# Kernel optimization log

Measured on AMD Instinct MI355X. Metric: run time of the kernel, lower is better.

Reference implementation:

```python
import jax, jax.numpy as jnp
import numpy as np
from jax import lax

B, H, W = 8, 512, 512


def setup_inputs() -> dict:
    key = jax.random.key(0)
    k1, k2, k3, k4, k5 = jax.random.split(key, 5)
    img = jax.random.uniform(k1, (B, 3, H, W), jnp.float32)
    omega = 0.8 + 0.15 * jax.random.uniform(k2, (B, 1), jnp.float32)
    atmospheric_light = 0.5 + 0.5 * jax.random.uniform(k3, (B, 3), jnp.float32)
    L_low = 2.0 * jax.random.uniform(k4, (B, 1), jnp.float32)          # percent in [0,2)
    L_high = 95.0 + 4.0 * jax.random.uniform(k5, (B, 1), jnp.float32)  # percent in [95,99)
    guided_radius = 15  # python int, uniform across batch (original clamps to [1,50])
    return {"img": img, "omega": omega, "atmospheric_light": atmospheric_light,
            "L_low": L_low, "L_high": L_high, "guided_radius": guided_radius}


def _box_filter(x, r):
    # reflect-pad + mean over (2r+1)x(2r+1) window, separable (exactly avg_pool2d on reflect-padded input)
    k = 2 * r + 1
    xp = jnp.pad(x, ((0, 0), (0, 0), (r, r), (r, r)), mode='reflect')
    s = lax.reduce_window(xp, 0.0, lax.add, (1, 1, k, 1), (1, 1, 1, 1), 'VALID')
    s = lax.reduce_window(s, 0.0, lax.add, (1, 1, 1, k), (1, 1, 1, 1), 'VALID')
    return s / (k * k)


def _forward(img, omega, atmospheric_light, L_low, L_high, r):
    eps = 0.5
    Bb, Cc, Hh, Ww = img.shape
    A = atmospheric_light.reshape(Bb, 3, 1, 1)
    # initial transmission: t = 1 - omega * min_c(I/A)
    dark = jnp.min(img / (A + 1e-8), axis=1, keepdims=True)           # (B,1,H,W)
    t0 = 1.0 - omega.reshape(Bb, 1, 1, 1) * dark
    # gradient constraint (weights from t0, applied to shifted copies)
    wx = jnp.exp(-jnp.abs(t0[:, :, :, 1:] - t0[:, :, :, :-1]))
    tx = jnp.concatenate([t0[:, :, :, :1], t0[:, :, :, :-1] * wx], axis=3)
    wy = jnp.exp(-jnp.abs(t0[:, :, 1:, :] - t0[:, :, :-1, :]))
    tg = jnp.concatenate([tx[:, :, :1, :], tx[:, :, :-1, :] * wy], axis=2)
    # guided filter with grayscale guide
    rgb_w = jnp.array([0.299, 0.587, 0.114], dtype=img.dtype).reshape(1, 3, 1, 1)
    gray = jnp.sum(img * rgb_w, axis=1, keepdims=True)                # (B,1,H,W)
    mI = _box_filter(gray, r)
    mp = _box_filter(tg, r)
    mIp = _box_filter(gray * tg, r)
    cov_Ip = mIp - mI * mp
    var_I = _box_filter(gray * gray, r) - mI * mI
    a = cov_Ip / (var_I + eps)
    b = mp - a * mI
    t_final = jnp.clip(_box_filter(a, r) * gray + _box_filter(b, r), 0.1, 1.0)
    # restoration
    J = jnp.clip((img - A) / (t_final + 1e-8) + A, 0.0, 1.0)
    # percentile color stretch (vectorized over B and C)
    n = Hh * Ww
    svals = jnp.sort(J.reshape(Bb, Cc, n), axis=-1)
    li = jnp.clip((L_low / 100.0 * n).astype(jnp.int32), 0, n - 1)    # (B,1)
    hi = jnp.clip((L_high / 100.0 * n).astype(jnp.int32), 0, n - 1)
    p_low = jnp.take_along_axis(svals, jnp.broadcast_to(li[:, :, None], (Bb, Cc, 1)), axis=-1).reshape(Bb, Cc, 1, 1)
    p_high = jnp.take_along_axis(svals, jnp.broadcast_to(hi[:, :, None], (Bb, Cc, 1)), axis=-1).reshape(Bb, Cc, 1, 1)
    out = (jnp.clip(J, p_low, p_high) - p_low) / (p_high - p_low + 1e-8)
    return jnp.clip(out, 0.0, 1.0)


def reference(img, omega, atmospheric_light, L_low, L_high, guided_radius):
    r = max(1, min(int(guided_radius), 50))
    return _forward(img, omega, atmospheric_light, L_low, L_high, r)
```

## Files before the change

### kernel.cpp

```cpp
#include <hip/hip_runtime.h>
#include <cstdint>

constexpr int Bb = 8, Hh = 512, Ww = 512;
constexpr int HWn = Hh * Ww;
constexpr int CHK2 = 16;
constexpr int CHK4 = 16;
constexpr int NBIN = 2048;

__device__ __forceinline__ int reflect_idx(int p, int n) {
    p = (p < 0) ? -p : p;
    return (p < n) ? p : (2 * n - 2 - p);
}
__device__ __forceinline__ int clamp_r(const int* rad) {
    int r = rad[0];
    return (r < 1) ? 1 : ((r > 50) ? 50 : r);
}

__global__ __launch_bounds__(512) void k1_stats_h(
    const float* __restrict__ img, const float* __restrict__ omega,
    const float* __restrict__ atm, const int* __restrict__ rad,
    float4* __restrict__ hq, unsigned int* __restrict__ histzero)
{
    const int i = blockIdx.x;
    const int b = blockIdx.y;
    const int j = threadIdx.x;
    const int fbid = b * gridDim.x + i;
    if (fbid < 96) histzero[fbid * 512 + j] = 0u;
    const int r = clamp_r(rad);

    __shared__ float t0c[512], t0p[512];
    __shared__ float4 Pb[512];
    __shared__ float4 wsum[8];

    const float om = omega[b];
    const float iA0 = 1.0f / (atm[b*3+0] + 1e-8f);
    const float iA1 = 1.0f / (atm[b*3+1] + 1e-8f);
    const float iA2 = 1.0f / (atm[b*3+2] + 1e-8f);
    const float* imb = img + (size_t)b * 3 * HWn;
    const int ip = (i > 0) ? (i - 1) : 0;

    float r0 = imb[0*HWn + i*Ww + j];
    float g0 = imb[1*HWn + i*Ww + j];
    float b0 = imb[2*HWn + i*Ww + j];
    t0c[j] = 1.0f - om * fminf(fminf(r0*iA0, g0*iA1), b0*iA2);
    float r1 = imb[0*HWn + ip*Ww + j];
    float g1 = imb[1*HWn + ip*Ww + j];
    float b1 = imb[2*HWn + ip*Ww + j];
    t0p[j] = 1.0f - om * fminf(fminf(r1*iA0, g1*iA1), b1*iA2);
    float gr = 0.299f*r0 + 0.587f*g0 + 0.114f*b0;
    __syncthreads();

    float tx = (j == 0) ? t0p[0] : t0p[j-1] * __expf(-fabsf(t0p[j] - t0p[j-1]));
    float tgv = (i == 0) ? tx : tx * __expf(-fabsf(t0c[j] - t0p[j]));

    const int lane = j & 63, wv = j >> 6;
    float4 incl;
    incl.x = gr; incl.y = tgv; incl.z = gr * tgv; incl.w = gr * gr;
    #pragma unroll
    for (int off = 1; off < 64; off <<= 1) {
        float ux = __shfl_up(incl.x, off);
        float uy = __shfl_up(incl.y, off);
        float uz = __shfl_up(incl.z, off);
        float uw = __shfl_up(incl.w, off);
        if (lane >= off) { incl.x += ux; incl.y += uy; incl.z += uz; incl.w += uw; }
    }
    if (lane == 63) wsum[wv] = incl;
    __syncthreads();
    float4 o4; o4.x = 0.f; o4.y = 0.f; o4.z = 0.f; o4.w = 0.f;
    #pragma unroll
    for (int w = 0; w < 7; ++w) {
        if (w < wv) {
            float4 t = wsum[w];
            o4.x += t.x; o4.y += t.y; o4.z += t.z; o4.w += t.w;
        }
    }
    float4 P; P.x = incl.x + o4.x; P.y = incl.y + o4.y; P.z = incl.z + o4.z; P.w = incl.w + o4.w;
    Pb[j] = P;
    __syncthreads();

    const int lo = j - r, hi = j + r;
    float4 s = Pb[(hi > 511) ? 511 : hi];
    if (lo > 0) {
        float4 t = Pb[lo-1];
        s.x -= t.x; s.y -= t.y; s.z -= t.z; s.w -= t.w;
    }
    if (lo < 0) {
        float4 t = Pb[r - j], u = Pb[0];
        s.x += t.x - u.x; s.y += t.y - u.y; s.z += t.z - u.z; s.w += t.w - u.w;
    }
    if (hi > 511) {
        float4 t = Pb[510], u = Pb[1021 - j - r];
        s.x += t.x - u.x; s.y += t.y - u.y; s.z += t.z - u.z; s.w += t.w - u.w;
    }
    hq[((size_t)b * Hh + i) * Ww + j] = s;
}

__global__ __launch_bounds__(256) void k2_stats_v(
    const float4* __restrict__ hq, const int* __restrict__ rad,
    float2* __restrict__ ab)
{
    const int b  = blockIdx.y;
    const int y0 = blockIdx.x * CHK2;
    const int j  = blockIdx.z * 256 + threadIdx.x;
    const int r  = clamp_r(rad);
    const float ikk = 1.0f / (float)((2*r+1) * (2*r+1));

    float4 s; s.x = 0.f; s.y = 0.f; s.z = 0.f; s.w = 0.f;
    for (int d = -r; d <= r; ++d) {
        int m = reflect_idx(y0 + d, Hh);
        float4 v = hq[((size_t)b * Hh + m) * Ww + j];
        s.x += v.x; s.y += v.y; s.z += v.z; s.w += v.w;
    }
    for (int y = y0; y < y0 + CHK2; ++y) {
        float mI = s.x * ikk, mp = s.y * ikk, mIp = s.z * ikk, mII = s.w * ikk;
        float av = (mIp - mI * mp) / (mII - mI * mI + 0.5f);
        float bv = mp - av * mI;
        float2 o; o.x = av; o.y = bv;
        ab[((size_t)b * Hh + y) * Ww + j] = o;
        int yin  = reflect_idx(y + 1 + r, Hh);
        int yout = reflect_idx(y - r, Hh);
        float4 vi = hq[((size_t)b * Hh + yin)  * Ww + j];
        float4 vo = hq[((size_t)b * Hh + yout) * Ww + j];
        s.x += vi.x - vo.x; s.y += vi.y - vo.y; s.z += vi.z - vo.z; s.w += vi.w - vo.w;
    }
}

__global__ __launch_bounds__(512) void k3_ab_h(
    const float2* __restrict__ ab, const int* __restrict__ rad,
    float2* __restrict__ hab)
{
    const int i = blockIdx.x;
    const int b = blockIdx.y;
    const int j = threadIdx.x;
    const int r = clamp_r(rad);
    const int lane = j & 63, wv = j >> 6;

    __shared__ float2 Pb[512];
    __shared__ float2 wsum[8];

    float2 v = ab[((size_t)b * Hh + i) * Ww + j];
    float2 incl = v;
    #pragma unroll
    for (int off = 1; off < 64; off <<= 1) {
        float ux = __shfl_up(incl.x, off);
        float uy = __shfl_up(incl.y, off);
        if (lane >= off) { incl.x += ux; incl.y += uy; }
    }
    if (lane == 63) wsum[wv] = incl;
    __syncthreads();
    float ox = 0.f, oy = 0.f;
    #pragma unroll
    for (int w = 0; w < 7; ++w) {
        if (w < wv) { float2 t = wsum[w]; ox += t.x; oy += t.y; }
    }
    float2 P; P.x = incl.x + ox; P.y = incl.y + oy;
    Pb[j] = P;
    __syncthreads();

    const int lo = j - r, hi = j + r;
    float2 s = Pb[(hi > 511) ? 511 : hi];
    if (lo > 0)   { float2 t = Pb[lo-1];  s.x -= t.x; s.y -= t.y; }
    if (lo < 0)   { float2 t = Pb[r-j], u = Pb[0];
                    s.x += t.x - u.x; s.y += t.y - u.y; }
    if (hi > 511) { float2 t = Pb[510], u = Pb[1021-j-r];
                    s.x += t.x - u.x; s.y += t.y - u.y; }
    hab[((size_t)b * Hh + i) * Ww + j] = s;
}

__global__ __launch_bounds__(256) void k4_final_v(
    const float2* __restrict__ hab, const float* __restrict__ img,
    const float* __restrict__ atm, const int* __restrict__ rad,
    float* __restrict__ J, unsigned int* __restrict__ hist)
{
    const int b  = blockIdx.y;
    const int y0 = blockIdx.x * CHK4;
    const int j  = blockIdx.z * 256 + threadIdx.x;
    const int tid = threadIdx.x;
    const int r  = clamp_r(rad);
    const float ikk = 1.0f / (float)((2*r+1) * (2*r+1));

    __shared__ unsigned int lh[3][NBIN];
    for (int t = tid; t < 3 * NBIN; t += 256) ((unsigned int*)lh)[t] = 0u;
    __syncthreads();

    float Aa[3];
    Aa[0] = atm[b*3+0]; Aa[1] = atm[b*3+1]; Aa[2] = atm[b*3+2];
    const float* imb = img + (size_t)b * 3 * HWn;
    float* Jb = J + (size_t)b * 3 * HWn;

    float2 V; V.x = 0.f; V.y = 0.f;
    for (int d = -r; d <= r; ++d) {
        int m = reflect_idx(y0 + d, Hh);
        float2 v = hab[((size_t)b * Hh + m) * Ww + j];
        V.x += v.x; V.y += v.y;
    }
    unsigned int clo[3] = {0u,0u,0u}, chi[3] = {0u,0u,0u};

    for (int y = y0; y < y0 + CHK4; ++y) {
        const size_t po = (size_t)y * Ww + j;
        float cc[3];
        cc[0] = imb[0*HWn + po]; cc[1] = imb[1*HWn + po]; cc[2] = imb[2*HWn + po];
        float g = 0.299f*cc[0] + 0.587f*cc[1] + 0.114f*cc[2];
        float t = fminf(fmaxf((V.x * g + V.y) * ikk, 0.1f), 1.0f);
        float invt = 1.0f / (t + 1e-8f);
        #pragma unroll
        for (int c = 0; c < 3; ++c) {
            float v = fminf(fmaxf((cc[c] - Aa[c]) * invt + Aa[c], 0.f), 1.f);
            Jb[c*HWn + po] = v;
            int bin = (int)(v * (float)NBIN);
            bin = (bin > NBIN-1) ? NBIN-1 : bin;
            if (bin == 0)            clo[c]++;
            else if (bin == NBIN-1)  chi[c]++;
            else atomicAdd(&lh[c][bin], 1u);
        }
        int yin  = reflect_idx(y + 1 + r, Hh);
        int yout = reflect_idx(y - r, Hh);
        float2 vi = hab[((size_t)b * Hh + yin)  * Ww + j];
        float2 vo = hab[((size_t)b * Hh + yout) * Ww + j];
        V.x += vi.x - vo.x; V.y += vi.y - vo.y;
    }
    #pragma unroll
    for (int c = 0; c < 3; ++c) {
        if (clo[c]) atomicAdd(&lh[c][0], clo[c]);
        if (chi[c]) atomicAdd(&lh[c][NBIN-1], chi[c]);
    }
    __syncthreads();
    for (int t = tid; t < 3 * NBIN; t += 256) {
        unsigned int v = ((unsigned int*)lh)[t];
        if (v) atomicAdd(&hist[(size_t)b * 3 * NBIN + t], v);
    }
}

__global__ __launch_bounds__(64) void k5_decide(
    const unsigned int* __restrict__ hist,
    const float* __restrict__ L_low, const float* __restrict__ L_high,
    float* __restrict__ p_low, float* __restrict__ p_high)
{
    const int t  = blockIdx.x / 24;
    const int bc = blockIdx.x % 24;
    const int b  = bc / 3;
    const int lane = threadIdx.x;
    const unsigned int* hb = hist + (size_t)bc * NBIN;

    unsigned int loc[NBIN / 64];
    unsigned int lsum = 0;
    #pragma unroll
    for (int i = 0; i < NBIN / 64; ++i) { loc[i] = hb[lane * (NBIN/64) + i]; lsum += loc[i]; }

    unsigned int incl = lsum;
    #pragma unroll
    for (int off = 1; off < 64; off <<= 1) {
        unsigned int v = __shfl_up(incl, off);
        if (lane >= off) incl += v;
    }
    unsigned int excl = incl - lsum;

    float L = t ? L_high[b] : L_low[b];
    int k = (int)(L * (1.0f / 100.0f) * (float)HWn);
    k = (k < 0) ? 0 : ((k > HWn - 1) ? HWn - 1 : k);

    if ((unsigned int)k >= excl && (unsigned int)k < incl) {
        unsigned int c = excl;
        #pragma unroll
        for (int i = 0; i < NBIN / 64; ++i) {
            if ((unsigned int)k < c + loc[i]) {
                float val = ((float)(lane * (NBIN/64) + i) + 0.5f) * (1.0f / (float)NBIN);
                if (t) p_high[bc] = val;
                else   p_low[bc]  = val;
                break;
            }
            c += loc[i];
        }
    }
}

__global__ __launch_bounds__(256) void k6_norm(
    float4* __restrict__ J,
    const float* __restrict__ p_low, const float* __restrict__ p_high)
{
    size_t idx = (size_t)blockIdx.x * 256 + threadIdx.x;
    int bc = (int)(idx >> 16);
    float l = p_low[bc], h = p_high[bc];
    float inv = 1.0f / (h - l + 1e-8f);
    float4 v = J[idx];
    v.x = fminf(fmaxf((fminf(fmaxf(v.x, l), h) - l) * inv, 0.f), 1.f);
    v.y = fminf(fmaxf((fminf(fmaxf(v.y, l), h) - l) * inv, 0.f), 1.f);
    v.z = fminf(fmaxf((fminf(fmaxf(v.z, l), h) - l) * inv, 0.f), 1.f);
    v.w = fminf(fmaxf((fminf(fmaxf(v.w, l), h) - l) * inv, 0.f), 1.f);
    J[idx] = v;
}

extern "C" void kernel_launch(void* const* d_in, const int* in_sizes, int n_in,
                              void* d_out, int out_size, void* d_ws, size_t ws_size,
                              hipStream_t stream)
{
    const float* img    = (const float*)d_in[0];
    const float* omega  = (const float*)d_in[1];
    const float* atm    = (const float*)d_in[2];
    const float* L_low  = (const float*)d_in[3];
    const float* L_high = (const float*)d_in[4];
    const int*   rad    = (const int*)d_in[5];
    float* J  = (float*)d_out;
    float* ws = (float*)d_ws;

    const size_t F = (size_t)Bb * HWn;
    float4* hq  = (float4*)ws;
    float2* ab  = (float2*)(ws + 4 * F);
    float2* hab = (float2*)ws;
    unsigned int* hist = (unsigned int*)(ws + 6 * F);
    float* pl = (float*)(hist + 24 * NBIN);
    float* ph = pl + 32;

    k1_stats_h<<<dim3(Hh, Bb), 512, 0, stream>>>(img, omega, atm, rad, hq, hist);
    k2_stats_v<<<dim3(Hh/CHK2, Bb, 2), 256, 0, stream>>>(hq, rad, ab);
    k3_ab_h   <<<dim3(Hh, Bb), 512, 0, stream>>>(ab, rad, hab);
    k4_final_v<<<dim3(Hh/CHK4, Bb, 2), 256, 0, stream>>>(hab, img, atm, rad, J, hist);
    k5_decide <<<48, 64, 0, stream>>>(hist, L_low, L_high, pl, ph);
    k6_norm   <<<(int)(3 * F / 4 / 256), 256, 0, stream>>>((float4*)J, pl, ph);
}
```

Measured before the change: 182.0 us.

## Fuse vertical stats and horizontal ab box filter; move histogram to separate pass

Merges the vertical running-sum kernel that computes a,b with the horizontal prefix-sum box filter, so each 512-wide block processes 8 rows and writes the horizontally filtered a,b directly. This drops the intermediate ab buffer round trip and one launch. The histogram is taken out of the final vertical kernel and done by a new pass over J with 1024 bins and 32 sub-blocks per channel, which cuts LDS use and atomic contention in k4 but adds a full extra read of J. Halving the bin count lowers percentile resolution, and the fused kernel has fewer blocks with two barriers per row.

```diff
diff --git a/kernel.cpp b/kernel.cpp
--- a/kernel.cpp
+++ b/kernel.cpp
@@ -3,9 +3,10 @@
 
 constexpr int Bb = 8, Hh = 512, Ww = 512;
 constexpr int HWn = Hh * Ww;
-constexpr int CHK2 = 16;
+constexpr int CH23 = 8;
 constexpr int CHK4 = 16;
-constexpr int NBIN = 2048;
+constexpr int NBIN = 1024;
+constexpr int NSUB = 32;
 
 __device__ __forceinline__ int reflect_idx(int p, int n) {
     p = (p < 0) ? -p : p;
@@ -25,7 +26,7 @@
     const int b = blockIdx.y;
     const int j = threadIdx.x;
     const int fbid = b * gridDim.x + i;
-    if (fbid < 96) histzero[fbid * 512 + j] = 0u;
+    if (fbid < 48) histzero[fbid * 512 + j] = 0u;
     const int r = clamp_r(rad);
 
     __shared__ float t0c[512], t0p[512];
@@ -95,15 +96,19 @@
     hq[((size_t)b * Hh + i) * Ww + j] = s;
 }
 
-__global__ __launch_bounds__(256) void k2_stats_v(
+__global__ __launch_bounds__(512) void k23_ab_h(
     const float4* __restrict__ hq, const int* __restrict__ rad,
-    float2* __restrict__ ab)
+    float2* __restrict__ hab)
 {
     const int b  = blockIdx.y;
-    const int y0 = blockIdx.x * CHK2;
-    const int j  = blockIdx.z * 256 + threadIdx.x;
+    const int y0 = blockIdx.x * CH23;
+    const int j  = threadIdx.x;
     const int r  = clamp_r(rad);
     const float ikk = 1.0f / (float)((2*r+1) * (2*r+1));
+    const int lane = j & 63, wv = j >> 6;
+
+    __shared__ float2 Pb[512];
+    __shared__ float2 wsum[8];
 
     float4 s; s.x = 0.f; s.y = 0.f; s.z = 0.f; s.w = 0.f;
     for (int d = -r; d <= r; ++d) {
@@ -111,12 +116,39 @@
         float4 v = hq[((size_t)b * Hh + m) * Ww + j];
         s.x += v.x; s.y += v.y; s.z += v.z; s.w += v.w;
     }
-    for (int y = y0; y < y0 + CHK2; ++y) {
+
+    for (int y = y0; y < y0 + CH23; ++y) {
         float mI = s.x * ikk, mp = s.y * ikk, mIp = s.z * ikk, mII = s.w * ikk;
         float av = (mIp - mI * mp) / (mII - mI * mI + 0.5f);
         float bv = mp - av * mI;
-        float2 o; o.x = av; o.y = bv;
-        ab[((size_t)b * Hh + y) * Ww + j] = o;
+
+        float2 incl; incl.x = av; incl.y = bv;
+        #pragma unroll
+        for (int off = 1; off < 64; off <<= 1) {
+            float ux = __shfl_up(incl.x, off);
+            float uy = __shfl_up(incl.y, off);
+            if (lane >= off) { incl.x += ux; incl.y += uy; }
+        }
+        if (lane == 63) wsum[wv] = incl;
+        __syncthreads();
+        float ox = 0.f, oy = 0.f;
+        #pragma unroll
+        for (int w = 0; w < 7; ++w) {
+            if (w < wv) { float2 t = wsum[w]; ox += t.x; oy += t.y; }
+        }
+        float2 P; P.x = incl.x + ox; P.y = incl.y + oy;
+        Pb[j] = P;
+        __syncthreads();
+
+        const int lo = j - r, hi = j + r;
+        float2 hs = Pb[(hi > 511) ? 511 : hi];
+        if (lo > 0)   { float2 t = Pb[lo-1];  hs.x -= t.x; hs.y -= t.y; }
+        if (lo < 0)   { float2 t = Pb[r-j], u = Pb[0];
+                        hs.x += t.x - u.x; hs.y += t.y - u.y; }
+        if (hi > 511) { float2 t = Pb[510], u = Pb[1021-j-r];
+                        hs.x += t.x - u.x; hs.y += t.y - u.y; }
+        hab[((size_t)b * Hh + y) * Ww + j] = hs;
+
         int yin  = reflect_idx(y + 1 + r, Hh);
         int yout = reflect_idx(y - r, Hh);
         float4 vi = hq[((size_t)b * Hh + yin)  * Ww + j];
@@ -125,63 +157,16 @@
     }
 }
 
-__global__ __launch_bounds__(512) void k3_ab_h(
-    const float2* __restrict__ ab, const int* __restrict__ rad,
-    float2* __restrict__ hab)
-{
-    const int i = blockIdx.x;
-    const int b = blockIdx.y;
-    const int j = threadIdx.x;
-    const int r = clamp_r(rad);
-    const int lane = j & 63, wv = j >> 6;
-
-    __shared__ float2 Pb[512];
-    __shared__ float2 wsum[8];
-
-    float2 v = ab[((size_t)b * Hh + i) * Ww + j];
-    float2 incl = v;
-    #pragma unroll
-    for (int off = 1; off < 64; off <<= 1) {
-        float ux = __shfl_up(incl.x, off);
-        float uy = __shfl_up(incl.y, off);
-        if (lane >= off) { incl.x += ux; incl.y += uy; }
-    }
-    if (lane == 63) wsum[wv] = incl;
-    __syncthreads();
-    float ox = 0.f, oy = 0.f;
-    #pragma unroll
-    for (int w = 0; w < 7; ++w) {
-        if (w < wv) { float2 t = wsum[w]; ox += t.x; oy += t.y; }
-    }
-    float2 P; P.x = incl.x + ox; P.y = incl.y + oy;
-    Pb[j] = P;
-    __syncthreads();
-
-    const int lo = j - r, hi = j + r;
-    float2 s = Pb[(hi > 511) ? 511 : hi];
-    if (lo > 0)   { float2 t = Pb[lo-1];  s.x -= t.x; s.y -= t.y; }
-    if (lo < 0)   { float2 t = Pb[r-j], u = Pb[0];
-                    s.x += t.x - u.x; s.y += t.y - u.y; }
-    if (hi > 511) { float2 t = Pb[510], u = Pb[1021-j-r];
-                    s.x += t.x - u.x; s.y += t.y - u.y; }
-    hab[((size_t)b * Hh + i) * Ww + j] = s;
-}
-
 __global__ __launch_bounds__(256) void k4_final_v(
     const float2* __restrict__ hab, const float* __restrict__ img,
     const float* __restrict__ atm, const int* __restrict__ rad,
-    float* __restrict__ J, unsigned int* __restrict__ hist)
+    float* __restrict__ J)
 {
     const int b  = blockIdx.y;
     const int y0 = blockIdx.x * CHK4;
     const int j  = blockIdx.z * 256 + threadIdx.x;
-    const int tid = threadIdx.x;
     const int r  = clamp_r(rad);
     const float ikk = 1.0f / (float)((2*r+1) * (2*r+1));
-
-    __shared__ unsigned int lh[3][NBIN];
-    for (int t = tid; t < 3 * NBIN; t += 256) ((unsigned int*)lh)[t] = 0u;
-    __syncthreads();
 
     float Aa[3];
     Aa[0] = atm[b*3+0]; Aa[1] = atm[b*3+1]; Aa[2] = atm[b*3+2];
@@ -194,7 +179,6 @@
         float2 v = hab[((size_t)b * Hh + m) * Ww + j];
         V.x += v.x; V.y += v.y;
     }
-    unsigned int clo[3] = {0u,0u,0u}, chi[3] = {0u,0u,0u};
 
     for (int y = y0; y < y0 + CHK4; ++y) {
         const size_t po = (size_t)y * Ww + j;
@@ -207,11 +191,6 @@
         for (int c = 0; c < 3; ++c) {
             float v = fminf(fmaxf((cc[c] - Aa[c]) * invt + Aa[c], 0.f), 1.f);
             Jb[c*HWn + po] = v;
-            int bin = (int)(v * (float)NBIN);
-            bin = (bin > NBIN-1) ? NBIN-1 : bin;
-            if (bin == 0)            clo[c]++;
-            else if (bin == NBIN-1)  chi[c]++;
-            else atomicAdd(&lh[c][bin], 1u);
         }
         int yin  = reflect_idx(y + 1 + r, Hh);
         int yout = reflect_idx(y - r, Hh);
@@ -219,15 +198,38 @@
         float2 vo = hab[((size_t)b * Hh + yout) * Ww + j];
         V.x += vi.x - vo.x; V.y += vi.y - vo.y;
     }
-    #pragma unroll
-    for (int c = 0; c < 3; ++c) {
-        if (clo[c]) atomicAdd(&lh[c][0], clo[c]);
-        if (chi[c]) atomicAdd(&lh[c][NBIN-1], chi[c]);
-    }
-    __syncthreads();
-    for (int t = tid; t < 3 * NBIN; t += 256) {
-        unsigned int v = ((unsigned int*)lh)[t];
-        if (v) atomicAdd(&hist[(size_t)b * 3 * NBIN + t], v);
+}
+
+__global__ __launch_bounds__(256) void k5_hist(
+    const float4* __restrict__ J, unsigned int* __restrict__ hist)
+{
+    const int bc  = blockIdx.x >> 5;
+    const int sub = blockIdx.x & (NSUB - 1);
+    const int tid = threadIdx.x;
+    __shared__ unsigned int lh[NBIN];
+    for (int i = tid; i < NBIN; i += 256) lh[i] = 0u;
+    __syncthreads();
+
+    const float4* base = J + (size_t)bc * (HWn / 4) + (size_t)sub * (HWn / 4 / NSUB);
+    unsigned int clo = 0, chi = 0;
+    for (int i = tid; i < HWn / 4 / NSUB; i += 256) {
+        float4 v = base[i];
+        #pragma unroll
+        for (int c = 0; c < 4; ++c) {
+            float f = (c == 0) ? v.x : (c == 1) ? v.y : (c == 2) ? v.z : v.w;
+            int bin = (int)(f * (float)NBIN);
+            bin = (bin > NBIN-1) ? NBIN-1 : bin;
+            if (bin == 0)           clo++;
+            else if (bin == NBIN-1) chi++;
+            else atomicAdd(&lh[bin], 1u);
+        }
+    }
+    if (clo) atomicAdd(&lh[0], clo);
+    if (chi) atomicAdd(&lh[NBIN-1], chi);
+    __syncthreads();
+    for (int i = tid; i < NBIN; i += 256) {
+        unsigned int v = lh[i];
+        if (v) atomicAdd(&hist[(size_t)bc * NBIN + i], v);
     }
 }
 
@@ -305,16 +307,15 @@
 
     const size_t F = (size_t)Bb * HWn;
     float4* hq  = (float4*)ws;
-    float2* ab  = (float2*)(ws + 4 * F);
-    float2* hab = (float2*)ws;
+    float2* hab = (float2*)(ws + 4 * F);
     unsigned int* hist = (unsigned int*)(ws + 6 * F);
     float* pl = (float*)(hist + 24 * NBIN);
     float* ph = pl + 32;
 
     k1_stats_h<<<dim3(Hh, Bb), 512, 0, stream>>>(img, omega, atm, rad, hq, hist);
-    k2_stats_v<<<dim3(Hh/CHK2, Bb, 2), 256, 0, stream>>>(hq, rad, ab);
-    k3_ab_h   <<<dim3(Hh, Bb), 512, 0, stream>>>(ab, rad, hab);
-    k4_final_v<<<dim3(Hh/CHK4, Bb, 2), 256, 0, stream>>>(hab, img, atm, rad, J, hist);
+    k23_ab_h  <<<dim3(Hh/CH23, Bb), 512, 0, stream>>>(hq, rad, hab);
+    k4_final_v<<<dim3(Hh/CHK4, Bb, 2), 256, 0, stream>>>(hab, img, atm, rad, J);
+    k5_hist   <<<24 * NSUB, 256, 0, stream>>>((const float4*)J, hist);
     k5_decide <<<48, 64, 0, stream>>>(hist, L_low, L_high, pl, ph);
     k6_norm   <<<(int)(3 * F / 4 / 256), 256, 0, stream>>>((float4*)J, pl, ph);
 }
```

New measurement: 167.9 us. -7.7%, faster.
